# Kernel optimization log

Measured on AMD Instinct MI355X. Metric: run time of the kernel, lower is better.

## Reference

```python
import jax, jax.numpy as jnp
import numpy as np

BUCKET_SIZE = 512
# Classic perfect-spatial-hashing primes (PSH / Teschner et al.)
P1 = np.uint32(73856093)
P2 = np.uint32(19349663)
P3 = np.uint32(83492791)
P4 = np.uint32(2654435761)  # mixes batch id into the hash


def setup_inputs() -> dict:
    key = jax.random.key(0)
    k1, k2 = jax.random.split(key)
    N, B = 4_000_000, 16
    coords = jax.random.normal(k1, (N, 3), dtype=jnp.float32) * 10.0
    seps = jnp.sort(jax.random.randint(k2, (B,), 0, N, dtype=jnp.int32))
    return {"coords": coords, "seps": seps, "hash_op": 1}


def reference(coords, seps, hash_op):
    """Hash-based bucket scatter with padding (PSHScatterLayer forward).

    Each point is voxelized, spatially hashed (mixed with its batch id from
    `seps`) into one of num_buckets buckets; points are written into a padded
    [pad_to, 3] buffer at slot = bucket * BUCKET_SIZE + within-bucket rank.
    Points overflowing a bucket are dropped (finite-capacity bucket counter).
    Deterministic rank (arrival order) replaces the CUDA atomic counter.
    """
    N = coords.shape[0]
    pad_to = ((N + BUCKET_SIZE - 1) // BUCKET_SIZE) * BUCKET_SIZE
    num_buckets = pad_to // BUCKET_SIZE

    # voxelize + spatial hash (non-differentiable index path)
    vox = jnp.floor(jax.lax.stop_gradient(coords)).astype(jnp.int32).astype(jnp.uint32)  # [N,3]
    batch_id = jnp.searchsorted(seps, jnp.arange(N, dtype=seps.dtype), side='right').astype(jnp.uint32)
    h = (vox[:, 0] * P1) ^ (vox[:, 1] * P2) ^ (vox[:, 2] * P3) ^ (batch_id * P4)
    h = h + jnp.uint32(hash_op)
    bucket = (h % jnp.uint32(num_buckets)).astype(jnp.int32)  # [N]

    # per-bucket counts and within-bucket rank (stable order = arrival order)
    counts = jax.ops.segment_sum(jnp.ones((N,), jnp.int32), bucket, num_segments=num_buckets)
    starts = jnp.cumsum(counts) - counts                      # [num_buckets]
    order = jnp.argsort(bucket)                               # stable in jax
    rank_sorted = jnp.arange(N, dtype=jnp.int32) - starts[bucket[order]]
    rank = jnp.zeros((N,), jnp.int32).at[order].set(rank_sorted)

    slot = bucket * BUCKET_SIZE + rank
    idx = jnp.where(rank < BUCKET_SIZE, slot, pad_to)         # out-of-range -> dropped
    scattered_coord = jnp.zeros((pad_to, 3), coords.dtype).at[idx].set(coords, mode='drop')
    return scattered_coord, counts, bucket
```

## Files before the change

### kernel.cpp

```cpp
#include <hip/hip_runtime.h>
#include <stdint.h>

#define PR1 73856093u
#define PR2 19349663u
#define PR3 83492791u
#define PR4 2654435761u
#define GS  32
#define PPT 4
#define BBITS 13

__device__ __forceinline__ uint32_t fastmod(uint32_t h, uint32_t d, double inv) {
    uint32_t q = (uint32_t)((double)h * inv);
    int32_t r = (int32_t)(h - q * d);
    if (r >= (int32_t)d) r -= d;
    if (r < 0) r += d;
    return (uint32_t)r;
}

__device__ __forceinline__ int chunk_of(int bi, int C) {
    return ((C & 7) == 0) ? ((bi & 7) * (C >> 3) + (bi >> 3)) : bi;
}

__global__ void k_bucket_hist(const float* __restrict__ coords,
                              const int* __restrict__ seps, int B,
                              const int* __restrict__ hash_op_p,
                              int N, int NB, int C, int chunk, double invNB,
                              float* __restrict__ out_bucket,
                              uint16_t* __restrict__ ch) {
    extern __shared__ int hist[];
    __shared__ int s_seps[1024];
    const int tid = threadIdx.x;
    for (int i = tid; i < NB; i += blockDim.x) hist[i] = 0;
    const int Bc = B < 1024 ? B : 1024;
    for (int j = tid; j < Bc; j += blockDim.x) s_seps[j] = seps[j];
    __syncthreads();

    const uint32_t hop = (uint32_t)hash_op_p[0];
    const int c = chunk_of(blockIdx.x, C);
    const int start = c * chunk;
    const int end   = min(start + chunk, N);
    int bid = 0;
    for (int i = start + tid; i < end; i += blockDim.x) {
        while (bid < B) {
            const int sv = (bid < 1024) ? s_seps[bid] : seps[bid];
            if (sv <= i) bid++; else break;
        }
        const float x = coords[3 * (size_t)i + 0];
        const float y = coords[3 * (size_t)i + 1];
        const float z = coords[3 * (size_t)i + 2];
        const uint32_t vx = (uint32_t)(int32_t)floorf(x);
        const uint32_t vy = (uint32_t)(int32_t)floorf(y);
        const uint32_t vz = (uint32_t)(int32_t)floorf(z);
        uint32_t h = vx * PR1 ^ vy * PR2 ^ vz * PR3 ^ ((uint32_t)bid * PR4);
        h += hop;
        const uint32_t b = fastmod(h, (uint32_t)NB, invNB);
        out_bucket[i] = (float)b;
        atomicAdd(&hist[(int)b], 1);
    }
    __syncthreads();
    uint16_t* dst = ch + (size_t)c * NB;
    for (int i = tid; i < NB; i += blockDim.x) dst[i] = (uint16_t)hist[i];
}

__global__ void k_scan_group(uint16_t* __restrict__ ch, int* __restrict__ Sg,
                             int C, int NB) {
    const int b = blockIdx.x * blockDim.x + threadIdx.x;
    if (b >= NB) return;
    const int g  = blockIdx.y;
    const int c0 = g * GS;
    const int c1 = min(c0 + GS, C);
    int run = 0;
    for (int c = c0; c < c1; c++) {
        const size_t idx = (size_t)c * NB + b;
        const int v = ch[idx];
        ch[idx] = (uint16_t)(run < 512 ? run : 512);
        run += v;
    }
    Sg[(size_t)g * NB + b] = run;
}

__global__ void k_scan_tops(int* __restrict__ Sg, int G, int NB,
                            float* __restrict__ out_counts,
                            float* __restrict__ out_sc) {
    const int b = blockIdx.x * blockDim.x + threadIdx.x;
    if (b >= NB) return;
    int run = 0;
    for (int g = 0; g < G; g++) {
        const size_t idx = (size_t)g * NB + b;
        const int v = Sg[idx];
        Sg[idx] = run;
        run += v;
    }
    out_counts[b] = (float)run;
    const int c0 = run < 512 ? run : 512;
    float* p = out_sc + ((size_t)b * 512 + c0) * 3;
    for (int j = c0; j < 512; j++) {
        p[0] = 0.f; p[1] = 0.f; p[2] = 0.f;
        p += 3;
    }
}

__global__ __launch_bounds__(256, 4)
void k_scatter(const float* __restrict__ coords,
               const float* __restrict__ bucket_f,
               const uint16_t* __restrict__ ch,
               const int* __restrict__ Sg,
               int N, int NB, int C, int chunk,
               float* __restrict__ out_sc) {
    extern __shared__ int hist[];
    const int tid = threadIdx.x;
    const int c = chunk_of(blockIdx.x, C);
    const int g = c / GS;
    const uint16_t* r1 = ch + (size_t)c * NB;
    const int*      r2 = Sg + (size_t)g * NB;
    for (int i = tid; i < NB; i += blockDim.x) hist[i] = (int)r1[i] + r2[i];
    __syncthreads();

    const int start = c * chunk;
    const int end   = min(start + chunk, N);
    const int len   = end > start ? end - start : 0;
    const int per_round = (int)blockDim.x * PPT;
    const int rounds = (len + per_round - 1) / per_round;
    const int lane = tid & 63;
    const int wv   = tid >> 6;
    const int nw   = (int)blockDim.x >> 6;
    const unsigned long long ltmask = ((unsigned long long)1 << lane) - 1;

    for (int rd = 0; rd < rounds; rd++) {
        const int wbase = start + rd * per_round + wv * (64 * PPT);
        int bs[PPT], leader[PPT], cntv[PPT], rnk[PPT];
        float cx[PPT], cy[PPT], cz[PPT];

        #pragma unroll
        for (int s = 0; s < PPT; s++) {
            const int i = wbase + s * 64 + lane;
            const bool v = (i < end);
            bs[s] = v ? (int)bucket_f[i] : NB;
            cx[s] = v ? coords[3 * (size_t)i + 0] : 0.f;
            cy[s] = v ? coords[3 * (size_t)i + 1] : 0.f;
            cz[s] = v ? coords[3 * (size_t)i + 2] : 0.f;
        }

        #pragma unroll
        for (int s = 0; s < PPT; s++) {
            const int b = bs[s];
            unsigned long long mm = ~0ull;
            #pragma unroll
            for (int k = 0; k < BBITS; k++) {
                const unsigned long long blt = __ballot(((b >> k) & 1) != 0);
                mm &= ((b >> k) & 1) ? blt : ~blt;
            }
            leader[s] = (int)__builtin_ctzll(mm);
            cntv[s]   = (int)__builtin_popcountll(mm);
            rnk[s]    = (int)__builtin_popcountll(mm & ltmask);
        }

        int basev[PPT];
        for (int w = 0; w < nw; w++) {
            if (wv == w) {
                #pragma unroll
                for (int s = 0; s < PPT; s++) {
                    int old = 0;
                    if (bs[s] < NB && lane == leader[s])
                        old = atomicAdd(&hist[bs[s]], cntv[s]);
                    basev[s] = __shfl(old, leader[s], 64);
                }
            }
            __syncthreads();
        }

        #pragma unroll
        for (int s = 0; s < PPT; s++) {
            if (bs[s] < NB) {
                const int r = basev[s] + rnk[s];
                if (r < 512) {
                    float* p = out_sc + ((size_t)bs[s] * 512 + r) * 3;
                    p[0] = cx[s]; p[1] = cy[s]; p[2] = cz[s];
                }
            }
        }
    }
}

extern "C" void kernel_launch(void* const* d_in, const int* in_sizes, int n_in,
                              void* d_out, int out_size, void* d_ws, size_t ws_size,
                              hipStream_t stream) {
    const float* coords  = (const float*)d_in[0];
    const int*   seps    = (const int*)d_in[1];
    const int*   hash_op = (const int*)d_in[2];

    const int N = in_sizes[0] / 3;
    const int B = in_sizes[1];
    const int pad_to = ((N + 511) / 512) * 512;
    const int NB = pad_to / 512;

    float* out        = (float*)d_out;
    float* out_counts = out + (size_t)pad_to * 3;
    float* out_bucket = out_counts + NB;

    int C = 1024;
    while (C > 8) {
        const int G_ = (C + GS - 1) / GS;
        if ((size_t)C * NB * 2 + (size_t)G_ * NB * 4 <= ws_size) break;
        C -= 8;
    }
    const int G = (C + GS - 1) / GS;
    const int chunk = (N + C - 1) / C;
    uint16_t* ch = (uint16_t*)d_ws;
    int* Sg = (int*)((char*)d_ws + (((size_t)C * NB * 2 + 15) & ~(size_t)15));
    const size_t lds = (size_t)NB * sizeof(int);
    const double invNB = 1.0 / (double)NB;

    k_bucket_hist<<<C, 256, lds, stream>>>(coords, seps, B, hash_op, N, NB, C,
                                           chunk, invNB, out_bucket, ch);
    dim3 g2a((NB + 255) / 256, G);
    k_scan_group<<<g2a, 256, 0, stream>>>(ch, Sg, C, NB);
    k_scan_tops<<<(NB + 255) / 256, 256, 0, stream>>>(Sg, G, NB, out_counts, out);
    k_scatter<<<C, 256, lds, stream>>>(coords, out_bucket, ch, Sg,
                                       N, NB, C, chunk, out);
}
```

Before: 217.4 us.

## Replace coordinate scatter with index permutation plus coalesced gather pass

The scatter kernel now writes only source point indices into a permutation buffer, and the padding slots are marked -1. A new gather kernel then walks output slots in order, reads coordinates through the permutation, and writes the padded output with coalesced stores, zero-filling empty slots. This replaces scattered 12-byte writes and the per-bucket zero-fill loop, at the cost of an extra kernel launch and an extra 4-byte-per-slot buffer pass. The chunk interleaving (chunk_of) is also removed, so blocks now process contiguous chunks in launch order.

```diff
diff --git a/kernel.cpp b/kernel.cpp
--- a/kernel.cpp
+++ b/kernel.cpp
@@ -17,14 +17,10 @@
     return (uint32_t)r;
 }
 
-__device__ __forceinline__ int chunk_of(int bi, int C) {
-    return ((C & 7) == 0) ? ((bi & 7) * (C >> 3) + (bi >> 3)) : bi;
-}
-
 __global__ void k_bucket_hist(const float* __restrict__ coords,
                               const int* __restrict__ seps, int B,
                               const int* __restrict__ hash_op_p,
-                              int N, int NB, int C, int chunk, double invNB,
+                              int N, int NB, int chunk, double invNB,
                               float* __restrict__ out_bucket,
                               uint16_t* __restrict__ ch) {
     extern __shared__ int hist[];
@@ -36,7 +32,7 @@
     __syncthreads();
 
     const uint32_t hop = (uint32_t)hash_op_p[0];
-    const int c = chunk_of(blockIdx.x, C);
+    const int c = blockIdx.x;
     const int start = c * chunk;
     const int end   = min(start + chunk, N);
     int bid = 0;
@@ -81,7 +77,7 @@
 
 __global__ void k_scan_tops(int* __restrict__ Sg, int G, int NB,
                             float* __restrict__ out_counts,
-                            float* __restrict__ out_sc) {
+                            int* __restrict__ perm, int pstride) {
     const int b = blockIdx.x * blockDim.x + threadIdx.x;
     if (b >= NB) return;
     int run = 0;
@@ -93,23 +89,19 @@
     }
     out_counts[b] = (float)run;
     const int c0 = run < 512 ? run : 512;
-    float* p = out_sc + ((size_t)b * 512 + c0) * 3;
-    for (int j = c0; j < 512; j++) {
-        p[0] = 0.f; p[1] = 0.f; p[2] = 0.f;
-        p += 3;
-    }
+    for (int j = c0; j < 512; j++)
+        perm[((size_t)b * 512 + j) * pstride] = -1;
 }
 
 __global__ __launch_bounds__(256, 4)
-void k_scatter(const float* __restrict__ coords,
-               const float* __restrict__ bucket_f,
-               const uint16_t* __restrict__ ch,
-               const int* __restrict__ Sg,
-               int N, int NB, int C, int chunk,
-               float* __restrict__ out_sc) {
+void k_perm(const float* __restrict__ bucket_f,
+            const uint16_t* __restrict__ ch,
+            const int* __restrict__ Sg,
+            int N, int NB, int chunk,
+            int* __restrict__ perm, int pstride) {
     extern __shared__ int hist[];
     const int tid = threadIdx.x;
-    const int c = chunk_of(blockIdx.x, C);
+    const int c = blockIdx.x;
     const int g = c / GS;
     const uint16_t* r1 = ch + (size_t)c * NB;
     const int*      r2 = Sg + (size_t)g * NB;
@@ -129,16 +121,11 @@
     for (int rd = 0; rd < rounds; rd++) {
         const int wbase = start + rd * per_round + wv * (64 * PPT);
         int bs[PPT], leader[PPT], cntv[PPT], rnk[PPT];
-        float cx[PPT], cy[PPT], cz[PPT];
 
         #pragma unroll
         for (int s = 0; s < PPT; s++) {
             const int i = wbase + s * 64 + lane;
-            const bool v = (i < end);
-            bs[s] = v ? (int)bucket_f[i] : NB;
-            cx[s] = v ? coords[3 * (size_t)i + 0] : 0.f;
-            cy[s] = v ? coords[3 * (size_t)i + 1] : 0.f;
-            cz[s] = v ? coords[3 * (size_t)i + 2] : 0.f;
+            bs[s] = (i < end) ? (int)bucket_f[i] : NB;
         }
 
         #pragma unroll
@@ -173,12 +160,35 @@
         for (int s = 0; s < PPT; s++) {
             if (bs[s] < NB) {
                 const int r = basev[s] + rnk[s];
-                if (r < 512) {
-                    float* p = out_sc + ((size_t)bs[s] * 512 + r) * 3;
-                    p[0] = cx[s]; p[1] = cy[s]; p[2] = cz[s];
-                }
+                if (r < 512)
+                    perm[((size_t)bs[s] * 512 + r) * pstride] =
+                        wbase + s * 64 + lane;
             }
         }
+    }
+}
+
+__global__ void k_gather(const int* __restrict__ perm, int pstride,
+                         const float* __restrict__ coords,
+                         int nslots, float* __restrict__ out_sc) {
+    const int base = blockIdx.x * (int)blockDim.x * PPT;
+    int idx[PPT];
+    #pragma unroll
+    for (int s = 0; s < PPT; s++) {
+        const int j = base + s * (int)blockDim.x + (int)threadIdx.x;
+        idx[s] = (j < nslots) ? perm[(size_t)j * pstride] : -2;
+    }
+    #pragma unroll
+    for (int s = 0; s < PPT; s++) {
+        const int j = base + s * (int)blockDim.x + (int)threadIdx.x;
+        if (idx[s] == -2) continue;
+        const bool v = (idx[s] >= 0);
+        const float* cp = coords + 3 * (size_t)(v ? idx[s] : 0);
+        const float x = v ? cp[0] : 0.f;
+        const float y = v ? cp[1] : 0.f;
+        const float z = v ? cp[2] : 0.f;
+        float* p = out_sc + 3 * (size_t)j;
+        p[0] = x; p[1] = y; p[2] = z;
     }
 }
 
@@ -198,24 +208,37 @@
     float* out_counts = out + (size_t)pad_to * 3;
     float* out_bucket = out_counts + NB;
 
+    const size_t permB = (((size_t)pad_to * 4) + 255) & ~(size_t)255;
+    int* perm; int pstride; char* wsrest; size_t wsrem;
+    if (ws_size > permB + (size_t)1024 * NB * 2 + (size_t)32 * NB * 4 + 256) {
+        perm = (int*)d_ws; pstride = 1;
+        wsrest = (char*)d_ws + permB; wsrem = ws_size - permB;
+    } else {
+        perm = (int*)out; pstride = 3;
+        wsrest = (char*)d_ws; wsrem = ws_size;
+    }
     int C = 1024;
     while (C > 8) {
         const int G_ = (C + GS - 1) / GS;
-        if ((size_t)C * NB * 2 + (size_t)G_ * NB * 4 <= ws_size) break;
+        if ((size_t)C * NB * 2 + (size_t)G_ * NB * 4 + 64 <= wsrem) break;
         C -= 8;
     }
     const int G = (C + GS - 1) / GS;
     const int chunk = (N + C - 1) / C;
-    uint16_t* ch = (uint16_t*)d_ws;
-    int* Sg = (int*)((char*)d_ws + (((size_t)C * NB * 2 + 15) & ~(size_t)15));
+    uint16_t* ch = (uint16_t*)wsrest;
+    int* Sg = (int*)(wsrest + (((size_t)C * NB * 2 + 15) & ~(size_t)15));
     const size_t lds = (size_t)NB * sizeof(int);
     const double invNB = 1.0 / (double)NB;
 
-    k_bucket_hist<<<C, 256, lds, stream>>>(coords, seps, B, hash_op, N, NB, C,
+    k_bucket_hist<<<C, 256, lds, stream>>>(coords, seps, B, hash_op, N, NB,
                                            chunk, invNB, out_bucket, ch);
     dim3 g2a((NB + 255) / 256, G);
     k_scan_group<<<g2a, 256, 0, stream>>>(ch, Sg, C, NB);
-    k_scan_tops<<<(NB + 255) / 256, 256, 0, stream>>>(Sg, G, NB, out_counts, out);
-    k_scatter<<<C, 256, lds, stream>>>(coords, out_bucket, ch, Sg,
-                                       N, NB, C, chunk, out);
-}
+    k_scan_tops<<<(NB + 255) / 256, 256, 0, stream>>>(Sg, G, NB, out_counts,
+                                                      perm, pstride);
+    k_perm<<<C, 256, lds, stream>>>(out_bucket, ch, Sg, N, NB, chunk,
+                                    perm, pstride);
+    const int slots_per_blk = 256 * PPT;
+    k_gather<<<(pad_to + slots_per_blk - 1) / slots_per_blk, 256, 0, stream>>>(
+        perm, pstride, coords, pad_to, out);
+}
```

Result: slower. 275.6 us (+26.8%).
